# Optimization experiments

Hardware: AMD Instinct MI355X
Metric: run time of the kernel (lower is better)

The kernel has to match this reference:

```python
import jax, jax.numpy as jnp
import numpy as np

J_NUM = 24
# SMPL kinematic tree: parents[i] < i for all i >= 1 (root has parent -1)
PARENTS = np.array([-1, 0, 0, 0, 1, 2, 3, 4, 5, 6, 7, 8, 9, 9, 9, 12, 13, 14,
                    16, 17, 18, 19, 20, 21], dtype=np.int32)
BATCH = 131072


def setup_inputs() -> dict:
    key = jax.random.key(0)
    k1, k2, k3 = jax.random.split(key, 3)
    pose = jax.random.normal(k1, (BATCH, J_NUM, 3), dtype=jnp.float32) * 0.3
    trans = jax.random.normal(k2, (BATCH, 3), dtype=jnp.float32)
    # Rest-pose joint transforms: identity rotation + random local offset (learned buffer)
    offs = jax.random.normal(k3, (J_NUM, 3), dtype=jnp.float32) * 0.1
    J = jnp.tile(jnp.eye(4, dtype=jnp.float32)[None], (J_NUM, 1, 1))
    J = J.at[:, :3, 3].set(offs)
    parents = jnp.asarray(PARENTS, dtype=jnp.int32)
    return {"pose": pose, "trans": trans, "J": J, "parents": parents}


def rodrigues(r):
    """Axis-angle [..., 3] -> rotation matrices [..., 3, 3] (batched Rodrigues)."""
    theta = jnp.sqrt(jnp.sum(r * r, axis=-1, keepdims=True) + 1e-16)  # [...,1]
    rh = r / theta
    x, y, z = rh[..., 0], rh[..., 1], rh[..., 2]
    zero = jnp.zeros_like(x)
    K = jnp.stack([zero, -z, y, z, zero, -x, -y, x, zero], axis=-1)
    K = K.reshape(r.shape[:-1] + (3, 3))
    c = jnp.cos(theta)[..., None]
    s = jnp.sin(theta)[..., None]
    outer = rh[..., :, None] * rh[..., None, :]
    I3 = jnp.eye(3, dtype=r.dtype)
    return c * I3 + (1.0 - c) * outer + s * K


def reference(pose, trans, J, parents):
    par = np.asarray(parents)  # static tree structure
    B, Jn = pose.shape[0], pose.shape[1]
    R = rodrigues(pose)                                   # [B,J,3,3]
    # embed into 4x4 homogeneous transforms
    R4 = jnp.pad(R, ((0, 0), (0, 0), (0, 1), (0, 1)))
    R4 = R4.at[:, :, 3, 3].set(1.0)                       # [B,J,4,4]
    # local transform per joint: J[i] @ localRot[i] (batched once)
    local = jnp.einsum('jab,njbc->njac', J, R4)           # [B,J,4,4]
    # sequential kinematic-tree composition (fixed small unrolled loop)
    results = [local[:, 0]]
    for i in range(1, Jn):
        results.append(jnp.matmul(results[int(par[i])], local[:, i]))
    stacked = jnp.stack(results, axis=1)                  # [B,J,4,4]
    J_posed = stacked[:, :, :3, 3] + trans[:, None, :]    # [B,J,3]
    return J_posed
```

## Files before the change

kernel.cpp:

```cpp
#include <hip/hip_runtime.h>

#define J_NUM 24
#define BLOCK 64
#define PSTRIDE 73
#define OSTRIDE 76
#define LDS_FLOATS (BLOCK * OSTRIDE)

__global__ __launch_bounds__(BLOCK, 2)
void fk_kernel(const float* __restrict__ pose, const float* __restrict__ trans,
               const float* __restrict__ Jm, float* __restrict__ out)
{
    __shared__ __align__(16) float s[LDS_FLOATS];

    const int t = threadIdx.x;
    const size_t blockBase = (size_t)blockIdx.x * BLOCK;
    const size_t b = blockBase + t;

    {
        const float4* src = reinterpret_cast<const float4*>(pose + blockBase * 72);
#pragma unroll
        for (int i = 0; i < 18; ++i) {
            int m = i * BLOCK + t;
            float4 v = src[m];
            int e = m / 18;
            int f = (m - e * 18) * 4;
            float* d = s + e * PSTRIDE + f;
            d[0] = v.x; d[1] = v.y; d[2] = v.z; d[3] = v.w;
        }
    }

    const float t0 = trans[b*3 + 0];
    const float t1 = trans[b*3 + 1];
    const float t2 = trans[b*3 + 2];

    __syncthreads();

    const float* p = s + t * PSTRIDE;

    const int par[J_NUM] = {-1,0,0,0,1,2,3,4,5,6,7,8,9,9,9,12,13,14,16,17,18,19,20,21};

    float Rc[J_NUM][9];
    float Pc[J_NUM][3];
    float o[72];

#pragma unroll
    for (int j = 0; j < J_NUM; ++j) {
        float ax = p[j*3+0], ay = p[j*3+1], az = p[j*3+2];
        float tt = fmaf(ax, ax, fmaf(ay, ay, fmaf(az, az, 1e-16f)));
        float inv = rsqrtf(tt);
        float th  = tt * inv;
        float x = ax*inv, y = ay*inv, z = az*inv;
        float c = __cosf(th), sn = __sinf(th);
        float C = 1.0f - c;
        float cx = C*x, cy = C*y, cz = C*z;
        float sx = sn*x, sy = sn*y, sz = sn*z;
        float R0 = fmaf(cx, x, c);
        float R1 = fmaf(cx, y, -sz);
        float R2 = fmaf(cx, z,  sy);
        float R3 = fmaf(cy, x,  sz);
        float R4 = fmaf(cy, y, c);
        float R5 = fmaf(cy, z, -sx);
        float R6 = fmaf(cz, x, -sy);
        float R7 = fmaf(cz, y,  sx);
        float R8 = fmaf(cz, z, c);

        float ox = Jm[j*16 + 3];
        float oy = Jm[j*16 + 7];
        float oz = Jm[j*16 + 11];

        if (j == 0) {
            Rc[0][0]=R0; Rc[0][1]=R1; Rc[0][2]=R2;
            Rc[0][3]=R3; Rc[0][4]=R4; Rc[0][5]=R5;
            Rc[0][6]=R6; Rc[0][7]=R7; Rc[0][8]=R8;
            Pc[0][0]=ox; Pc[0][1]=oy; Pc[0][2]=oz;
        } else {
            const int q = par[j];
            Pc[j][0] = fmaf(Rc[q][0], ox, fmaf(Rc[q][1], oy, fmaf(Rc[q][2], oz, Pc[q][0])));
            Pc[j][1] = fmaf(Rc[q][3], ox, fmaf(Rc[q][4], oy, fmaf(Rc[q][5], oz, Pc[q][1])));
            Pc[j][2] = fmaf(Rc[q][6], ox, fmaf(Rc[q][7], oy, fmaf(Rc[q][8], oz, Pc[q][2])));
            Rc[j][0] = fmaf(Rc[q][0], R0, fmaf(Rc[q][1], R3, Rc[q][2]*R6));
            Rc[j][1] = fmaf(Rc[q][0], R1, fmaf(Rc[q][1], R4, Rc[q][2]*R7));
            Rc[j][2] = fmaf(Rc[q][0], R2, fmaf(Rc[q][1], R5, Rc[q][2]*R8));
            Rc[j][3] = fmaf(Rc[q][3], R0, fmaf(Rc[q][4], R3, Rc[q][5]*R6));
            Rc[j][4] = fmaf(Rc[q][3], R1, fmaf(Rc[q][4], R4, Rc[q][5]*R7));
            Rc[j][5] = fmaf(Rc[q][3], R2, fmaf(Rc[q][4], R5, Rc[q][5]*R8));
            Rc[j][6] = fmaf(Rc[q][6], R0, fmaf(Rc[q][7], R3, Rc[q][8]*R6));
            Rc[j][7] = fmaf(Rc[q][6], R1, fmaf(Rc[q][7], R4, Rc[q][8]*R7));
            Rc[j][8] = fmaf(Rc[q][6], R2, fmaf(Rc[q][7], R5, Rc[q][8]*R8));
        }

        o[j*3+0] = Pc[j][0] + t0;
        o[j*3+1] = Pc[j][1] + t1;
        o[j*3+2] = Pc[j][2] + t2;
    }

    __syncthreads();

    {
        float* mine = s + t * OSTRIDE;
#pragma unroll
        for (int k = 0; k < 18; ++k) {
            float4 v;
            v.x = o[4*k+0]; v.y = o[4*k+1]; v.z = o[4*k+2]; v.w = o[4*k+3];
            *reinterpret_cast<float4*>(mine + 4*k) = v;
        }
    }

    __syncthreads();

    {
        float4* dst = reinterpret_cast<float4*>(out + blockBase * 72);
#pragma unroll
        for (int i = 0; i < 18; ++i) {
            int m = i * BLOCK + t;
            int e = m / 18;
            int f = (m - e * 18) * 4;
            float4 v = *reinterpret_cast<const float4*>(s + e * OSTRIDE + f);
            dst[m] = v;
        }
    }
}

extern "C" void kernel_launch(void* const* d_in, const int* in_sizes, int n_in,
                              void* d_out, int out_size, void* d_ws, size_t ws_size,
                              hipStream_t stream) {
    const float* pose  = (const float*)d_in[0];
    const float* trans = (const float*)d_in[1];
    const float* Jm    = (const float*)d_in[2];
    float* out = (float*)d_out;

    int B = in_sizes[0] / (J_NUM * 3);
    int blocks = B / BLOCK;
    fk_kernel<<<blocks, BLOCK, 0, stream>>>(pose, trans, Jm, out);
}
```

Baseline: 93.13 us.

## Process two batch chunks per block with prefetch and wave-level barriers

Each 64-thread block now handles 128 elements. It prefetches the second chunk's pose into registers while the first chunk is computed, which overlaps global load latency with compute. Input and output now use separate LDS buffers, and __syncthreads is replaced with a waitcnt plus wave barrier, which is valid because the block is a single wave. In exchange, register pressure rises from the 72 extra floats held for the prefetch, the launch-bounds occupancy hint is dropped, LDS use per block roughly doubles, and the grid is half as large.

```diff
diff --git a/kernel.cpp b/kernel.cpp
--- a/kernel.cpp
+++ b/kernel.cpp
@@ -4,45 +4,19 @@
 #define BLOCK 64
 #define PSTRIDE 73
 #define OSTRIDE 76
-#define LDS_FLOATS (BLOCK * OSTRIDE)
+#define EPB 128
 
-__global__ __launch_bounds__(BLOCK, 2)
-void fk_kernel(const float* __restrict__ pose, const float* __restrict__ trans,
-               const float* __restrict__ Jm, float* __restrict__ out)
+#define WAVE_SYNC() do { asm volatile("s_waitcnt lgkmcnt(0)" ::: "memory"); \
+                         __builtin_amdgcn_wave_barrier(); } while (0)
+
+__device__ __forceinline__ void compute_elem(const float* __restrict__ p,
+                                             const float* __restrict__ Jm,
+                                             float t0, float t1, float t2,
+                                             float* __restrict__ o)
 {
-    __shared__ __align__(16) float s[LDS_FLOATS];
-
-    const int t = threadIdx.x;
-    const size_t blockBase = (size_t)blockIdx.x * BLOCK;
-    const size_t b = blockBase + t;
-
-    {
-        const float4* src = reinterpret_cast<const float4*>(pose + blockBase * 72);
-#pragma unroll
-        for (int i = 0; i < 18; ++i) {
-            int m = i * BLOCK + t;
-            float4 v = src[m];
-            int e = m / 18;
-            int f = (m - e * 18) * 4;
-            float* d = s + e * PSTRIDE + f;
-            d[0] = v.x; d[1] = v.y; d[2] = v.z; d[3] = v.w;
-        }
-    }
-
-    const float t0 = trans[b*3 + 0];
-    const float t1 = trans[b*3 + 1];
-    const float t2 = trans[b*3 + 2];
-
-    __syncthreads();
-
-    const float* p = s + t * PSTRIDE;
-
     const int par[J_NUM] = {-1,0,0,0,1,2,3,4,5,6,7,8,9,9,9,12,13,14,16,17,18,19,20,21};
-
     float Rc[J_NUM][9];
     float Pc[J_NUM][3];
-    float o[72];
-
 #pragma unroll
     for (int j = 0; j < J_NUM; ++j) {
         float ax = p[j*3+0], ay = p[j*3+1], az = p[j*3+2];
@@ -93,30 +67,102 @@
         o[j*3+1] = Pc[j][1] + t1;
         o[j*3+2] = Pc[j][2] + t2;
     }
+}
 
-    __syncthreads();
+__global__ __launch_bounds__(BLOCK)
+void fk_kernel(const float* __restrict__ pose, const float* __restrict__ trans,
+               const float* __restrict__ Jm, float* __restrict__ out)
+{
+    __shared__ __align__(16) float sp[BLOCK * PSTRIDE];
+    __shared__ __align__(16) float so[BLOCK * OSTRIDE];
+
+    const int t = threadIdx.x;
+    const size_t base = (size_t)blockIdx.x * EPB;
+    const size_t b0 = base + t;
+    const size_t b1 = base + 64 + t;
+
+    float4 L0[18];
+    {
+        const float4* src = reinterpret_cast<const float4*>(pose + base * 72);
+#pragma unroll
+        for (int i = 0; i < 18; ++i) L0[i] = src[i * BLOCK + t];
+    }
+    const float a0 = trans[b0*3+0], a1 = trans[b0*3+1], a2 = trans[b0*3+2];
+
+#pragma unroll
+    for (int i = 0; i < 18; ++i) {
+        int m = i * BLOCK + t;
+        int e = m / 18;
+        int f = (m - e * 18) * 4;
+        float* d = sp + e * PSTRIDE + f;
+        d[0] = L0[i].x; d[1] = L0[i].y; d[2] = L0[i].z; d[3] = L0[i].w;
+    }
+
+    float4 L1[18];
+    {
+        const float4* src = reinterpret_cast<const float4*>(pose + (base + 64) * 72);
+#pragma unroll
+        for (int i = 0; i < 18; ++i) L1[i] = src[i * BLOCK + t];
+    }
+    const float c0 = trans[b1*3+0], c1 = trans[b1*3+1], c2 = trans[b1*3+2];
+
+    WAVE_SYNC();
+
+    float o0[72];
+    compute_elem(sp + t * PSTRIDE, Jm, a0, a1, a2, o0);
 
     {
-        float* mine = s + t * OSTRIDE;
+        float* mine = so + t * OSTRIDE;
 #pragma unroll
         for (int k = 0; k < 18; ++k) {
-            float4 v;
-            v.x = o[4*k+0]; v.y = o[4*k+1]; v.z = o[4*k+2]; v.w = o[4*k+3];
+            float4 v; v.x=o0[4*k+0]; v.y=o0[4*k+1]; v.z=o0[4*k+2]; v.w=o0[4*k+3];
             *reinterpret_cast<float4*>(mine + 4*k) = v;
         }
     }
-
-    __syncthreads();
+    WAVE_SYNC();
 
     {
-        float4* dst = reinterpret_cast<float4*>(out + blockBase * 72);
+        float4* dst = reinterpret_cast<float4*>(out + base * 72);
 #pragma unroll
         for (int i = 0; i < 18; ++i) {
             int m = i * BLOCK + t;
             int e = m / 18;
             int f = (m - e * 18) * 4;
-            float4 v = *reinterpret_cast<const float4*>(s + e * OSTRIDE + f);
-            dst[m] = v;
+            dst[m] = *reinterpret_cast<const float4*>(so + e * OSTRIDE + f);
+        }
+    }
+
+#pragma unroll
+    for (int i = 0; i < 18; ++i) {
+        int m = i * BLOCK + t;
+        int e = m / 18;
+        int f = (m - e * 18) * 4;
+        float* d = sp + e * PSTRIDE + f;
+        d[0] = L1[i].x; d[1] = L1[i].y; d[2] = L1[i].z; d[3] = L1[i].w;
+    }
+    WAVE_SYNC();
+
+    float o1[72];
+    compute_elem(sp + t * PSTRIDE, Jm, c0, c1, c2, o1);
+
+    {
+        float* mine = so + t * OSTRIDE;
+#pragma unroll
+        for (int k = 0; k < 18; ++k) {
+            float4 v; v.x=o1[4*k+0]; v.y=o1[4*k+1]; v.z=o1[4*k+2]; v.w=o1[4*k+3];
+            *reinterpret_cast<float4*>(mine + 4*k) = v;
+        }
+    }
+    WAVE_SYNC();
+
+    {
+        float4* dst = reinterpret_cast<float4*>(out + (base + 64) * 72);
+#pragma unroll
+        for (int i = 0; i < 18; ++i) {
+            int m = i * BLOCK + t;
+            int e = m / 18;
+            int f = (m - e * 18) * 4;
+            dst[m] = *reinterpret_cast<const float4*>(so + e * OSTRIDE + f);
         }
     }
 }
@@ -130,6 +176,6 @@
     float* out = (float*)d_out;
 
     int B = in_sizes[0] / (J_NUM * 3);
-    int blocks = B / BLOCK;
+    int blocks = B / EPB;
     fk_kernel<<<blocks, BLOCK, 0, stream>>>(pose, trans, Jm, out);
 }
```

New measurement: 95.63 us. 1.03x slower.
